# Kernel optimization log

Measured on AMD Instinct MI355X. Metric: run time of the kernel, lower is better.

## Reference

```python
import jax, jax.numpy as jnp
import numpy as np

N, DEG, FIN, HID, OUT = 50000, 16, 128, 128, 64


def setup_inputs() -> dict:
    key = jax.random.key(0)
    ks = jax.random.split(key, 32)
    x = jax.random.normal(ks[0], (N, FIN), dtype=jnp.float32)
    src = jax.random.randint(ks[1], (N * DEG,), 0, N, dtype=jnp.int32)
    dst = jnp.repeat(jnp.arange(N, dtype=jnp.int32), DEG)  # sorted by target, fixed degree
    edge_index = jnp.stack([src, dst])  # [2, E]
    dims = [(FIN, HID), (HID, HID), (HID, OUT)]
    params = {}
    i = 2
    for l, (fi, fo) in enumerate(dims, 1):
        s_lstm = 1.0 / np.sqrt(fi)
        params[f"W_ih{l}"] = jax.random.normal(ks[i + 0], (4 * fi, fi)) * s_lstm
        params[f"W_hh{l}"] = jax.random.normal(ks[i + 1], (4 * fi, fi)) * s_lstm
        params[f"b_ih{l}"] = jax.random.normal(ks[i + 2], (4 * fi,)) * s_lstm
        params[f"b_hh{l}"] = jax.random.normal(ks[i + 3], (4 * fi,)) * s_lstm
        params[f"Wl{l}"] = jax.random.normal(ks[i + 4], (fo, fi)) * (1.0 / np.sqrt(fi))
        params[f"bl{l}"] = jnp.zeros((fo,), jnp.float32)
        params[f"Wr{l}"] = jax.random.normal(ks[i + 5], (fo, fi)) * (1.0 / np.sqrt(fi))
        i += 6
    return {"x": x, "edge_index": edge_index, **params}


def _lstm_last(neigh, Wih, Whh, bih, bhh):
    # neigh: [N, deg, Fi]; PyTorch LSTM gate order i,f,g,o; return last-step output h.
    h0 = jnp.zeros((neigh.shape[0], Wih.shape[0] // 4), neigh.dtype)
    bias = bih + bhh

    def step(carry, xt):
        h, c = carry
        g = xt @ Wih.T + h @ Whh.T + bias
        i, f, gg, o = jnp.split(g, 4, axis=-1)
        c = jax.nn.sigmoid(f) * c + jax.nn.sigmoid(i) * jnp.tanh(gg)
        h = jax.nn.sigmoid(o) * jnp.tanh(c)
        return (h, c), None

    (h, _), _ = jax.lax.scan(step, (h0, h0), jnp.swapaxes(neigh, 0, 1))
    return h


def _sage_layer(x, src2d, Wih, Whh, bih, bhh, Wl, bl, Wr):
    neigh = x[src2d]  # gather: [N, deg, Fi]
    aggr = _lstm_last(neigh, Wih, Whh, bih, bhh)  # [N, Fi]
    return aggr @ Wl.T + bl + x @ Wr.T  # lin_l(aggr) + lin_r(x)


def reference(x, edge_index,
              W_ih1, W_hh1, b_ih1, b_hh1, Wl1, bl1, Wr1,
              W_ih2, W_hh2, b_ih2, b_hh2, Wl2, bl2, Wr2,
              W_ih3, W_hh3, b_ih3, b_hh3, Wl3, bl3, Wr3):
    n = x.shape[0]
    src2d = edge_index[0].reshape(n, -1)  # fixed-degree, dst-sorted edge list
    h = _sage_layer(x, src2d, W_ih1, W_hh1, b_ih1, b_hh1, Wl1, bl1, Wr1)
    h = jax.nn.relu(h)  # dropout is identity in eval mode
    h = _sage_layer(h, src2d, W_ih2, W_hh2, b_ih2, b_hh2, Wl2, bl2, Wr2)
    h = jax.nn.relu(h)
    return _sage_layer(h, src2d, W_ih3, W_hh3, b_ih3, b_hh3, Wl3, bl3, Wr3)
```

## Files before the change

### kernel.cpp

```cpp
#include <hip/hip_runtime.h>
#include <cstddef>
#include <cstdint>

typedef __attribute__((ext_vector_type(4))) float f32x4;
typedef __attribute__((ext_vector_type(8))) short short8;

#define HID 128
#define NK1 -1.4426950408889634f
#define PK2 2.8853900817779268f

#define BAR_LGKM() __asm__ volatile("s_waitcnt lgkmcnt(0)\ns_barrier" ::: "memory")
#define STEP_BAR2() __asm__ volatile("s_waitcnt vmcnt(2) lgkmcnt(0)\ns_barrier" ::: "memory")

__device__ __forceinline__ short f2bf(float f) {
  unsigned u = __builtin_bit_cast(unsigned, f);
  u += 0x7FFFu + ((u >> 16) & 1u);
  return (short)(u >> 16);
}
__device__ __forceinline__ unsigned pack_bf2(float a, float b) {
  unsigned ua = __builtin_bit_cast(unsigned, a) + 0x8000u;
  unsigned ub = __builtin_bit_cast(unsigned, b) + 0x8000u;
  return __builtin_amdgcn_perm(ub, ua, 0x07060302u);
}

__device__ __forceinline__ float lstm_elem(float si, float sf, float sg, float so, float& c) {
  float Ei = __builtin_amdgcn_exp2f(si);
  float Ef = __builtin_amdgcn_exp2f(sf);
  float Tg = __builtin_amdgcn_exp2f(sg);
  float Eo = __builtin_amdgcn_exp2f(so);
  float u = 1.0f + Ei, w = 1.0f + Ef, v = Tg + 1.0f, Tm = Tg - 1.0f;
  float t0 = u * v;
  float num = __builtin_fmaf(c, t0, w * Tm);
  float cn = num * __builtin_amdgcn_rcpf(w * t0);
  c = cn;
  float Tc = __builtin_amdgcn_exp2f(PK2 * cn);
  return (Tc - 1.0f) * __builtin_amdgcn_rcpf((1.0f + Eo) * (Tc + 1.0f));
}

__global__ void conv_x_kernel(const float* __restrict__ x, short* __restrict__ xb, int n,
                              int* __restrict__ tctr) {
  int i = blockIdx.x * blockDim.x + threadIdx.x;
  if (i < 8) tctr[i] = 0;
  int stride = gridDim.x * blockDim.x;
  for (; i < n; i += stride) xb[i] = f2bf(x[i]);
}

__global__ void conv_layer_kernel(const float* __restrict__ Wih, const float* __restrict__ Whh,
                                  const float* __restrict__ bih, const float* __restrict__ bhh,
                                  const float* __restrict__ Wl, const float* __restrict__ Wr, int foK,
                                  short* __restrict__ wihB, short* __restrict__ whhB,
                                  short* __restrict__ wlB, short* __restrict__ wrB,
                                  float* __restrict__ bsum) {
  int i = blockIdx.x * blockDim.x + threadIdx.x;
  if (i < 512 * HID) {
    float sc = ((i >> 14) == 2) ? PK2 : NK1;
    wihB[i] = f2bf(Wih[i] * sc);
    whhB[i] = f2bf(Whh[i] * sc);
  }
  if (i < foK) { wlB[i] = f2bf(Wl[i]); wrB[i] = f2bf(Wr[i]); }
  if (i < 512) bsum[i] = (bih[i] + bhh[i]) * (((i >> 7) == 2) ? PK2 : NK1);
}

#define ASTR 136
__global__ __launch_bounds__(512, 4) void pgemm_kernel(
    const short* __restrict__ A, const short* __restrict__ W,
    const float* __restrict__ bias, short* __restrict__ out, int M, int ntiles) {
  __shared__ short ldsA[32 * ASTR];
  const int tid = threadIdx.x;
  const int wave = tid >> 6, lane = tid & 63;
  const int quad = lane >> 4, nn = lane & 15;
  const int cbase = wave * 64;

  short8 wreg[4][4];
#pragma unroll
  for (int kt = 0; kt < 4; ++kt)
#pragma unroll
    for (int nt = 0; nt < 4; ++nt)
      wreg[kt][nt] = *(const short8*)(W + (size_t)(cbase + nt * 16 + nn) * HID + kt * 32 + quad * 8);
  f32x4 bias4[4];
#pragma unroll
  for (int nt = 0; nt < 4; ++nt)
#pragma unroll
    for (int r = 0; r < 4; ++r) bias4[nt][r] = bias[cbase + nt * 16 + quad * 4 + r];

  const int srow = wave * 4 + quad;
  const int scol = nn * 8;

  int rt = blockIdx.x;
  short8 avn;
  {
    int r = rt * 32 + srow;
    if (r > M - 1) r = M - 1;
    avn = *(const short8*)(A + (size_t)r * HID + scol);
  }

#pragma unroll 1
  for (; rt < ntiles; rt += gridDim.x) {
    const int row0 = rt * 32;
    BAR_LGKM();
    *(short8*)(ldsA + srow * ASTR + scol) = avn;
    {
      int rn = rt + gridDim.x;
      if (rn < ntiles) {
        int r = rn * 32 + srow;
        if (r > M - 1) r = M - 1;
        avn = *(const short8*)(A + (size_t)r * HID + scol);
      }
    }
    BAR_LGKM();

    f32x4 acc[2][4];
#pragma unroll
    for (int b = 0; b < 2; ++b)
#pragma unroll
      for (int nt = 0; nt < 4; ++nt) acc[b][nt] = bias4[nt];
#pragma unroll
    for (int kt = 0; kt < 4; ++kt) {
      short8 af0 = *(const short8*)(ldsA + nn * ASTR + kt * 32 + quad * 8);
      short8 af1 = *(const short8*)(ldsA + (16 + nn) * ASTR + kt * 32 + quad * 8);
#pragma unroll
      for (int nt = 0; nt < 4; ++nt) {
        acc[0][nt] = __builtin_amdgcn_mfma_f32_16x16x32_bf16(wreg[kt][nt], af0, acc[0][nt], 0, 0, 0);
        acc[1][nt] = __builtin_amdgcn_mfma_f32_16x16x32_bf16(wreg[kt][nt], af1, acc[1][nt], 0, 0, 0);
      }
    }

#pragma unroll
    for (int b = 0; b < 2; ++b) {
      int row = row0 + b * 16 + nn;
      if (row < M) {
#pragma unroll
        for (int nt = 0; nt < 4; ++nt) {
          uint2 pk;
          pk.x = pack_bf2(acc[b][nt][0], acc[b][nt][1]);
          pk.y = pack_bf2(acc[b][nt][2], acc[b][nt][3]);
          *(uint2*)(out + (size_t)row * 512 + cbase + nt * 16 + quad * 4) = pk;
        }
      }
    }
  }
}

#define NPB 16
#define PSTR 520
#define HSTR 152
#define LSTM_LDS_BYTES ((3 * NPB * PSTR + 2 * NPB * HSTR) * 2 + 256 * 4 + 16)

template <int FO, bool RELU, bool OUTF32>
__global__ __launch_bounds__(512, 4) void lstm_fused_kernel(
    const short* __restrict__ P, const short* __restrict__ Whh,
    const int* __restrict__ src, const short* __restrict__ cur,
    const short* __restrict__ Wl, const short* __restrict__ Wr,
    const float* __restrict__ bl,
    short* __restrict__ outB, float* __restrict__ outF, int M, int ntiles,
    int* __restrict__ tctr) {
  extern __shared__ char smem[];
  short* Pb = (short*)smem;
  short* Hb = Pb + 3 * NPB * PSTR;
  int* srcL = (int*)(Hb + 2 * NPB * HSTR);
  int* nextTp = srcL + 256;

  const int tid = threadIdx.x;
  const int wave = tid >> 6, lane = tid & 63;
  const int quad = lane >> 4, nn = lane & 15;
  const int r0row = wave * 2, r1row = wave * 2 + 1;
  const char* Pbase = (const char*)P + lane * 16;

  short8 wreg[4][4];
#pragma unroll
  for (int kt = 0; kt < 4; ++kt)
#pragma unroll
    for (int q = 0; q < 4; ++q)
      wreg[kt][q] = *(const short8*)(Whh + (size_t)(q * 128 + wave * 16 + nn) * HID + kt * 32 + quad * 8);

  short8 ident;
#pragma unroll
  for (int e = 0; e < 8; ++e) ident[e] = (short)((quad * 8 + e == nn) ? 0x3F80 : 0);
  f32x4 zero4 = {0.f, 0.f, 0.f, 0.f};
  __asm__ volatile("" : "+v"(zero4));

  int tile = blockIdx.x;
  while (tile < ntiles) {
    const int nodeBase = tile * NPB;
    if (tid < 256) {
      int node = nodeBase + (tid >> 4);
      srcL[tid] = ((node < M) ? src[nodeBase * 16 + tid] : 0) << 10;
    }
    if (tid == 0) *nextTp = (int)gridDim.x + atomicAdd(tctr, 1);
    float c_st[4] = {0.f, 0.f, 0.f, 0.f};
    BAR_LGKM();
    const int my_next = *nextTp;

    {
      int s0A = srcL[r0row * 16 + 0], s0B = srcL[r1row * 16 + 0];
      __builtin_amdgcn_global_load_lds(
          (const __attribute__((address_space(1))) unsigned int*)(Pbase + s0A),
          (__attribute__((address_space(3))) unsigned int*)(Pb + r0row * PSTR), 16, 0, 0);
      __builtin_amdgcn_global_load_lds(
          (const __attribute__((address_space(1))) unsigned int*)(Pbase + s0B),
          (__attribute__((address_space(3))) unsigned int*)(Pb + r1row * PSTR), 16, 0, 0);
      int s1A = srcL[r0row * 16 + 1], s1B = srcL[r1row * 16 + 1];
      __builtin_amdgcn_global_load_lds(
          (const __attribute__((address_space(1))) unsigned int*)(Pbase + s1A),
          (__attribute__((address_space(3))) unsigned int*)(Pb + NPB * PSTR + r0row * PSTR), 16, 0, 0);
      __builtin_amdgcn_global_load_lds(
          (const __attribute__((address_space(1))) unsigned int*)(Pbase + s1B),
          (__attribute__((address_space(3))) unsigned int*)(Pb + NPB * PSTR + r1row * PSTR), 16, 0, 0);
    }
    int sA = srcL[r0row * 16 + 2], sB = srcL[r1row * 16 + 2];

    int pc = 0, pg = 2;
#pragma unroll 1
    for (int t = 0; t < 16; ++t) {
      short* Pc = Pb + pc * NPB * PSTR;
      short* Pg = Pb + pg * NPB * PSTR;
      const short* Hp = Hb + ((t + 1) & 1) * NPB * HSTR;
      short* Hw = Hb + (t & 1) * NPB * HSTR;
      pc = (pc == 2) ? 0 : pc + 1;
      pg = (pg == 2) ? 0 : pg + 1;

      STEP_BAR2();

      const short* pB = Pc + nn * PSTR + wave * 16 + (quad & 1) * 8;
      short8 pf0 = *(const short8*)(pB + 0 * 128);
      short8 pf1 = *(const short8*)(pB + 1 * 128);
      short8 pf2 = *(const short8*)(pB + 2 * 128);
      short8 pf3 = *(const short8*)(pB + 3 * 128);

      __builtin_amdgcn_global_load_lds(
          (const __attribute__((address_space(1))) unsigned int*)(Pbase + sA),
          (__attribute__((address_space(3))) unsigned int*)(Pg + r0row * PSTR), 16, 0, 0);
      __builtin_amdgcn_global_load_lds(
          (const __attribute__((address_space(1))) unsigned int*)(Pbase + sB),
          (__attribute__((address_space(3))) unsigned int*)(Pg + r1row * PSTR), 16, 0, 0);
      {
        int tn = (t + 3 < 16) ? t + 3 : 15;
        sA = srcL[r0row * 16 + tn];
        sB = srcL[r1row * 16 + tn];
      }

      f32x4 acc[4];
      acc[0] = __builtin_amdgcn_mfma_f32_16x16x32_bf16(ident, pf0, zero4, 0, 0, 0);
      acc[1] = __builtin_amdgcn_mfma_f32_16x16x32_bf16(ident, pf1, zero4, 0, 0, 0);
      acc[2] = __builtin_amdgcn_mfma_f32_16x16x32_bf16(ident, pf2, zero4, 0, 0, 0);
      acc[3] = __builtin_amdgcn_mfma_f32_16x16x32_bf16(ident, pf3, zero4, 0, 0, 0);

      if (t) {
#pragma unroll
        for (int kt = 0; kt < 4; ++kt) {
          short8 hb = *(const short8*)(Hp + nn * HSTR + kt * 32 + quad * 8);
#pragma unroll
          for (int q = 0; q < 4; ++q)
            acc[q] = __builtin_amdgcn_mfma_f32_16x16x32_bf16(wreg[kt][q], hb, acc[q], 0, 0, 0);
        }
      }

      float hv[4];
#pragma unroll
      for (int r = 0; r < 4; ++r)
        hv[r] = lstm_elem(acc[0][r], acc[1][r], acc[2][r], acc[3][r], c_st[r]);
      uint2 pk;
      pk.x = pack_bf2(hv[0], hv[1]);
      pk.y = pack_bf2(hv[2], hv[3]);
      *(uint2*)(Hw + nn * HSTR + wave * 16 + quad * 4) = pk;
    }

    BAR_LGKM();

    if (FO == 128 || wave < 4) {
      const short* Hf = Hb + NPB * HSTR;
      const int cbase = wave * 16;
      f32x4 accO;
#pragma unroll
      for (int r = 0; r < 4; ++r) accO[r] = bl[cbase + quad * 4 + r];
#pragma unroll
      for (int kt = 0; kt < 4; ++kt) {
        short8 wlA = *(const short8*)(Wl + (size_t)(cbase + nn) * HID + kt * 32 + quad * 8);
        short8 hb = *(const short8*)(Hf + nn * HSTR + kt * 32 + quad * 8);
        accO = __builtin_amdgcn_mfma_f32_16x16x32_bf16(wlA, hb, accO, 0, 0, 0);
        short8 wrA = *(const short8*)(Wr + (size_t)(cbase + nn) * HID + kt * 32 + quad * 8);
        short8 cb = *(const short8*)(cur + (size_t)(nodeBase + nn) * HID + kt * 32 + quad * 8);
        accO = __builtin_amdgcn_mfma_f32_16x16x32_bf16(wrA, cb, accO, 0, 0, 0);
      }
      if (RELU) {
#pragma unroll
        for (int r = 0; r < 4; ++r) accO[r] = fmaxf(accO[r], 0.0f);
      }
      int node = nodeBase + nn;
      if (node < M) {
        if (OUTF32) {
          *(f32x4*)(outF + (size_t)node * FO + cbase + quad * 4) = accO;
        } else {
          uint2 pko;
          pko.x = pack_bf2(accO[0], accO[1]);
          pko.y = pack_bf2(accO[2], accO[3]);
          *(uint2*)(outB + (size_t)node * FO + cbase + quad * 4) = pko;
        }
      }
    }
    tile = my_next;
  }
}

extern "C" void kernel_launch(void* const* d_in, const int* in_sizes, int n_in,
                              void* d_out, int out_size, void* d_ws, size_t ws_size,
                              hipStream_t stream) {
  const float* x = (const float*)d_in[0];
  const int* src = (const int*)d_in[1];
  const float* Wih[3] = {(const float*)d_in[2], (const float*)d_in[9], (const float*)d_in[16]};
  const float* Whh[3] = {(const float*)d_in[3], (const float*)d_in[10], (const float*)d_in[17]};
  const float* bih[3] = {(const float*)d_in[4], (const float*)d_in[11], (const float*)d_in[18]};
  const float* bhh[3] = {(const float*)d_in[5], (const float*)d_in[12], (const float*)d_in[19]};
  const float* Wl[3]  = {(const float*)d_in[6], (const float*)d_in[13], (const float*)d_in[20]};
  const float* bl[3]  = {(const float*)d_in[7], (const float*)d_in[14], (const float*)d_in[21]};
  const float* Wr[3]  = {(const float*)d_in[8], (const float*)d_in[15], (const float*)d_in[22]};

  const int M = in_sizes[0] / HID;

  char* ws = (char*)d_ws;
  size_t off = 0;
  auto alloc = [&](size_t bytes) -> void* {
    void* p = ws + off;
    off += (bytes + 255) & ~(size_t)255;
    return p;
  };
  short* curA = (short*)alloc((size_t)M * HID * 2);
  short* curB = (short*)alloc((size_t)M * HID * 2);
  short* Pbuf = (short*)alloc((size_t)M * 512 * 2);
  short* wihB[3]; short* whhB[3]; short* wlB[3]; short* wrB[3]; float* bsum[3];
  for (int l = 0; l < 3; ++l) {
    wihB[l] = (short*)alloc(512 * HID * 2);
    whhB[l] = (short*)alloc(512 * HID * 2);
    wlB[l]  = (short*)alloc(HID * HID * 2);
    wrB[l]  = (short*)alloc(HID * HID * 2);
    bsum[l] = (float*)alloc(512 * 4);
  }
  int* tctr = (int*)alloc(256);

  const int nltiles = (M + NPB - 1) / NPB;
  const int ntiles = (M + 31) / 32;

  (void)hipFuncSetAttribute((const void*)lstm_fused_kernel<128, true, false>,
                            hipFuncAttributeMaxDynamicSharedMemorySize, LSTM_LDS_BYTES);
  (void)hipFuncSetAttribute((const void*)lstm_fused_kernel<64, false, true>,
                            hipFuncAttributeMaxDynamicSharedMemorySize, LSTM_LDS_BYTES);

  conv_x_kernel<<<2048, 256, 0, stream>>>(x, curA, M * HID, tctr);
  for (int l = 0; l < 3; ++l) {
    const int Fo = (l == 2) ? 64 : 128;
    conv_layer_kernel<<<256, 256, 0, stream>>>(Wih[l], Whh[l], bih[l], bhh[l], Wl[l], Wr[l],
                                               Fo * HID, wihB[l], whhB[l], wlB[l], wrB[l], bsum[l]);
  }

  short* cur = curA;
  short* nxt = curB;
  for (int l = 0; l < 3; ++l) {
    pgemm_kernel<<<784, 512, 0, stream>>>(cur, wihB[l], bsum[l], Pbuf, M, ntiles);
    if (l < 2) {
      lstm_fused_kernel<128, true, false><<<512, 512, LSTM_LDS_BYTES, stream>>>(
          Pbuf, whhB[l], src, cur, wlB[l], wrB[l], bl[l], nxt, nullptr, M, nltiles, tctr + l);
      short* tswap = cur; cur = nxt; nxt = tswap;
    } else {
      lstm_fused_kernel<64, false, true><<<512, 512, LSTM_LDS_BYTES, stream>>>(
          Pbuf, whhB[l], src, cur, wlB[l], wrB[l], bl[l], nullptr, (float*)d_out, M, nltiles, tctr + 2);
    }
  }
}
```

Before: 741.3 us.

## Fuse all conversion, GEMM and LSTM stages into one cooperative persistent kernel

Replaces the sequence of conversion, input-projection GEMM and fused LSTM kernel launches with a single cooperative kernel that uses grid-wide syncs between phases. The input GEMM phase also switches to atomic-counter dynamic tile scheduling and stages bias in LDS. The aim is to remove per-launch overhead and tail gaps between kernels. The cost is grid.sync overhead and grid size being tied to occupancy, with the old multi-kernel path kept as a fallback if the cooperative launch fails.

```diff
diff --git a/kernel.cpp b/kernel.cpp
--- a/kernel.cpp
+++ b/kernel.cpp
@@ -1,6 +1,9 @@
 #include <hip/hip_runtime.h>
+#include <hip/hip_cooperative_groups.h>
 #include <cstddef>
 #include <cstdint>
+
+namespace cg = cooperative_groups;
 
 typedef __attribute__((ext_vector_type(4))) float f32x4;
 typedef __attribute__((ext_vector_type(8))) short short8;
@@ -37,6 +40,296 @@
   return (Tc - 1.0f) * __builtin_amdgcn_rcpf((1.0f + Eo) * (Tc + 1.0f));
 }
 
+#define ASTR 136
+#define NPB 16
+#define PSTR 520
+#define HSTR 152
+#define LSTM_LDS_BYTES ((3 * NPB * PSTR + 2 * NPB * HSTR) * 2 + 256 * 4 + 16)
+
+struct KParams {
+  const float* x;
+  const int* src;
+  const float* Wih[3]; const float* Whh[3];
+  const float* bih[3]; const float* bhh[3];
+  const float* Wl[3];  const float* bl[3]; const float* Wr[3];
+  short* curA; short* curB; short* Pbuf;
+  short* wihB[3]; short* whhB[3]; short* wlB[3]; short* wrB[3];
+  float* bsum[3];
+  int* tctr;
+  float* outF;
+  int M, ntiles, nltiles;
+};
+
+__global__ __launch_bounds__(512, 4) void fused_all(KParams p) {
+  extern __shared__ char smem[];
+  const int tid = threadIdx.x;
+  const int wave = tid >> 6, lane = tid & 63;
+  const int quad = lane >> 4, nn = lane & 15;
+  cg::grid_group grid = cg::this_grid();
+
+  {
+    const int gi = blockIdx.x * 512 + tid;
+    const int gs = (int)gridDim.x * 512;
+    if (gi < 8) p.tctr[gi] = 0;
+    const int nx = p.M * HID;
+    for (int i = gi; i < nx; i += gs) p.curA[i] = f2bf(p.x[i]);
+#pragma unroll 1
+    for (int l = 0; l < 3; ++l) {
+      const int foK = ((l == 2) ? 64 : 128) * HID;
+      for (int i = gi; i < 512 * HID; i += gs) {
+        float sc = ((i >> 14) == 2) ? PK2 : NK1;
+        p.wihB[l][i] = f2bf(p.Wih[l][i] * sc);
+        p.whhB[l][i] = f2bf(p.Whh[l][i] * sc);
+      }
+      for (int i = gi; i < foK; i += gs) {
+        p.wlB[l][i] = f2bf(p.Wl[l][i]);
+        p.wrB[l][i] = f2bf(p.Wr[l][i]);
+      }
+      for (int i = gi; i < 512; i += gs)
+        p.bsum[l][i] = (p.bih[l][i] + p.bhh[l][i]) * (((i >> 7) == 2) ? PK2 : NK1);
+    }
+  }
+  grid.sync();
+
+  short* cur = p.curA;
+  short* nxt = p.curB;
+
+#pragma unroll 1
+  for (int l = 0; l < 3; ++l) {
+    {
+      short* ldsA = (short*)smem;
+      float* ldsB = (float*)(smem + 32 * ASTR * 2);
+      int* nextTp = (int*)(ldsB + 512);
+      const short* A = cur;
+      const short* W = p.wihB[l];
+      short* outP = p.Pbuf;
+      int* ctr = p.tctr + 3 + l;
+      const int Mloc = p.M, ntl = p.ntiles;
+      const int cbase = wave * 64;
+      const int srow = wave * 4 + quad;
+      const int scol = nn * 8;
+
+      short8 wreg[4][4];
+#pragma unroll
+      for (int kt = 0; kt < 4; ++kt)
+#pragma unroll
+        for (int nt = 0; nt < 4; ++nt)
+          wreg[kt][nt] = *(const short8*)(W + (size_t)(cbase + nt * 16 + nn) * HID + kt * 32 + quad * 8);
+      ldsB[tid] = p.bsum[l][tid];
+
+      int rt = blockIdx.x;
+      short8 avn;
+      {
+        int r = rt * 32 + srow;
+        if (r > Mloc - 1) r = Mloc - 1;
+        avn = *(const short8*)(A + (size_t)r * HID + scol);
+      }
+#pragma unroll 1
+      while (rt < ntl) {
+        if (tid == 0) *nextTp = (int)gridDim.x + atomicAdd(ctr, 1);
+        BAR_LGKM();
+        *(short8*)(ldsA + srow * ASTR + scol) = avn;
+        const int rn = *nextTp;
+        if (rn < ntl) {
+          int r = rn * 32 + srow;
+          if (r > Mloc - 1) r = Mloc - 1;
+          avn = *(const short8*)(A + (size_t)r * HID + scol);
+        }
+        BAR_LGKM();
+        f32x4 acc[2][4];
+#pragma unroll
+        for (int nt = 0; nt < 4; ++nt) {
+          f32x4 bv = *(const f32x4*)(ldsB + cbase + nt * 16 + quad * 4);
+          acc[0][nt] = bv;
+          acc[1][nt] = bv;
+        }
+#pragma unroll
+        for (int kt = 0; kt < 4; ++kt) {
+          short8 af0 = *(const short8*)(ldsA + nn * ASTR + kt * 32 + quad * 8);
+          short8 af1 = *(const short8*)(ldsA + (16 + nn) * ASTR + kt * 32 + quad * 8);
+#pragma unroll
+          for (int nt = 0; nt < 4; ++nt) {
+            acc[0][nt] = __builtin_amdgcn_mfma_f32_16x16x32_bf16(wreg[kt][nt], af0, acc[0][nt], 0, 0, 0);
+            acc[1][nt] = __builtin_amdgcn_mfma_f32_16x16x32_bf16(wreg[kt][nt], af1, acc[1][nt], 0, 0, 0);
+          }
+        }
+        const int row0 = rt * 32;
+#pragma unroll
+        for (int b = 0; b < 2; ++b) {
+          int row = row0 + b * 16 + nn;
+          if (row < Mloc) {
+#pragma unroll
+            for (int nt = 0; nt < 4; ++nt) {
+              uint2 pk;
+              pk.x = pack_bf2(acc[b][nt][0], acc[b][nt][1]);
+              pk.y = pack_bf2(acc[b][nt][2], acc[b][nt][3]);
+              *(uint2*)(outP + (size_t)row * 512 + cbase + nt * 16 + quad * 4) = pk;
+            }
+          }
+        }
+        rt = rn;
+      }
+    }
+    grid.sync();
+
+    {
+      short* Pb = (short*)smem;
+      short* Hb = Pb + 3 * NPB * PSTR;
+      int* srcL = (int*)(Hb + 2 * NPB * HSTR);
+      int* nextTp = srcL + 256;
+      const short* Whh = p.whhB[l];
+      const short* Wlw = p.wlB[l];
+      const short* Wrw = p.wrB[l];
+      const float* blw = p.bl[l];
+      int* ctr = p.tctr + l;
+      const int Mloc = p.M, ntl = p.nltiles;
+      const int r0row = wave * 2, r1row = wave * 2 + 1;
+      const char* Pbase = (const char*)p.Pbuf + lane * 16;
+      const int FO = (l == 2) ? 64 : 128;
+
+      short8 wreg[4][4];
+#pragma unroll
+      for (int kt = 0; kt < 4; ++kt)
+#pragma unroll
+        for (int q = 0; q < 4; ++q)
+          wreg[kt][q] = *(const short8*)(Whh + (size_t)(q * 128 + wave * 16 + nn) * HID + kt * 32 + quad * 8);
+
+      short8 ident;
+#pragma unroll
+      for (int e = 0; e < 8; ++e) ident[e] = (short)((quad * 8 + e == nn) ? 0x3F80 : 0);
+      f32x4 zero4 = {0.f, 0.f, 0.f, 0.f};
+      __asm__ volatile("" : "+v"(zero4));
+
+      int tile = blockIdx.x;
+#pragma unroll 1
+      while (tile < ntl) {
+        const int nodeBase = tile * NPB;
+        if (tid < 256) {
+          int node = nodeBase + (tid >> 4);
+          srcL[tid] = ((node < Mloc) ? p.src[nodeBase * 16 + tid] : 0) << 10;
+        }
+        if (tid == 0) *nextTp = (int)gridDim.x + atomicAdd(ctr, 1);
+        float c_st[4] = {0.f, 0.f, 0.f, 0.f};
+        BAR_LGKM();
+        const int my_next = *nextTp;
+
+        {
+          int s0A = srcL[r0row * 16 + 0], s0B = srcL[r1row * 16 + 0];
+          __builtin_amdgcn_global_load_lds(
+              (const __attribute__((address_space(1))) unsigned int*)(Pbase + s0A),
+              (__attribute__((address_space(3))) unsigned int*)(Pb + r0row * PSTR), 16, 0, 0);
+          __builtin_amdgcn_global_load_lds(
+              (const __attribute__((address_space(1))) unsigned int*)(Pbase + s0B),
+              (__attribute__((address_space(3))) unsigned int*)(Pb + r1row * PSTR), 16, 0, 0);
+          int s1A = srcL[r0row * 16 + 1], s1B = srcL[r1row * 16 + 1];
+          __builtin_amdgcn_global_load_lds(
+              (const __attribute__((address_space(1))) unsigned int*)(Pbase + s1A),
+              (__attribute__((address_space(3))) unsigned int*)(Pb + NPB * PSTR + r0row * PSTR), 16, 0, 0);
+          __builtin_amdgcn_global_load_lds(
+              (const __attribute__((address_space(1))) unsigned int*)(Pbase + s1B),
+              (__attribute__((address_space(3))) unsigned int*)(Pb + NPB * PSTR + r1row * PSTR), 16, 0, 0);
+        }
+        int sA = srcL[r0row * 16 + 2], sB = srcL[r1row * 16 + 2];
+
+        int pc = 0, pg = 2;
+#pragma unroll 1
+        for (int t = 0; t < 16; ++t) {
+          short* Pc = Pb + pc * NPB * PSTR;
+          short* Pg = Pb + pg * NPB * PSTR;
+          const short* Hp = Hb + ((t + 1) & 1) * NPB * HSTR;
+          short* Hw = Hb + (t & 1) * NPB * HSTR;
+          pc = (pc == 2) ? 0 : pc + 1;
+          pg = (pg == 2) ? 0 : pg + 1;
+
+          STEP_BAR2();
+
+          const short* pB = Pc + nn * PSTR + wave * 16 + (quad & 1) * 8;
+          short8 pf0 = *(const short8*)(pB + 0 * 128);
+          short8 pf1 = *(const short8*)(pB + 1 * 128);
+          short8 pf2 = *(const short8*)(pB + 2 * 128);
+          short8 pf3 = *(const short8*)(pB + 3 * 128);
+
+          __builtin_amdgcn_global_load_lds(
+              (const __attribute__((address_space(1))) unsigned int*)(Pbase + sA),
+              (__attribute__((address_space(3))) unsigned int*)(Pg + r0row * PSTR), 16, 0, 0);
+          __builtin_amdgcn_global_load_lds(
+              (const __attribute__((address_space(1))) unsigned int*)(Pbase + sB),
+              (__attribute__((address_space(3))) unsigned int*)(Pg + r1row * PSTR), 16, 0, 0);
+          {
+            int tn = (t + 3 < 16) ? t + 3 : 15;
+            sA = srcL[r0row * 16 + tn];
+            sB = srcL[r1row * 16 + tn];
+          }
+
+          f32x4 acc[4];
+          acc[0] = __builtin_amdgcn_mfma_f32_16x16x32_bf16(ident, pf0, zero4, 0, 0, 0);
+          acc[1] = __builtin_amdgcn_mfma_f32_16x16x32_bf16(ident, pf1, zero4, 0, 0, 0);
+          acc[2] = __builtin_amdgcn_mfma_f32_16x16x32_bf16(ident, pf2, zero4, 0, 0, 0);
+          acc[3] = __builtin_amdgcn_mfma_f32_16x16x32_bf16(ident, pf3, zero4, 0, 0, 0);
+
+          if (t) {
+#pragma unroll
+            for (int kt = 0; kt < 4; ++kt) {
+              short8 hb = *(const short8*)(Hp + nn * HSTR + kt * 32 + quad * 8);
+#pragma unroll
+              for (int q = 0; q < 4; ++q)
+                acc[q] = __builtin_amdgcn_mfma_f32_16x16x32_bf16(wreg[kt][q], hb, acc[q], 0, 0, 0);
+            }
+          }
+
+          float hv[4];
+#pragma unroll
+          for (int r = 0; r < 4; ++r)
+            hv[r] = lstm_elem(acc[0][r], acc[1][r], acc[2][r], acc[3][r], c_st[r]);
+          uint2 pk;
+          pk.x = pack_bf2(hv[0], hv[1]);
+          pk.y = pack_bf2(hv[2], hv[3]);
+          *(uint2*)(Hw + nn * HSTR + wave * 16 + quad * 4) = pk;
+        }
+
+        BAR_LGKM();
+
+        if (FO == 128 || wave < 4) {
+          const short* Hf = Hb + NPB * HSTR;
+          const int cbase = wave * 16;
+          f32x4 accO;
+#pragma unroll
+          for (int r = 0; r < 4; ++r) accO[r] = blw[cbase + quad * 4 + r];
+#pragma unroll
+          for (int kt = 0; kt < 4; ++kt) {
+            short8 wlA = *(const short8*)(Wlw + (size_t)(cbase + nn) * HID + kt * 32 + quad * 8);
+            short8 hb = *(const short8*)(Hf + nn * HSTR + kt * 32 + quad * 8);
+            accO = __builtin_amdgcn_mfma_f32_16x16x32_bf16(wlA, hb, accO, 0, 0, 0);
+            short8 wrA = *(const short8*)(Wrw + (size_t)(cbase + nn) * HID + kt * 32 + quad * 8);
+            short8 cb = *(const short8*)(cur + (size_t)(nodeBase + nn) * HID + kt * 32 + quad * 8);
+            accO = __builtin_amdgcn_mfma_f32_16x16x32_bf16(wrA, cb, accO, 0, 0, 0);
+          }
+          if (l < 2) {
+#pragma unroll
+            for (int r = 0; r < 4; ++r) accO[r] = fmaxf(accO[r], 0.0f);
+          }
+          int node = nodeBase + nn;
+          if (node < Mloc) {
+            if (l == 2) {
+              *(f32x4*)(p.outF + (size_t)node * 64 + cbase + quad * 4) = accO;
+            } else {
+              uint2 pko;
+              pko.x = pack_bf2(accO[0], accO[1]);
+              pko.y = pack_bf2(accO[2], accO[3]);
+              *(uint2*)(nxt + (size_t)node * 128 + cbase + quad * 4) = pko;
+            }
+          }
+        }
+        tile = my_next;
+      }
+    }
+    if (l < 2) {
+      grid.sync();
+      short* t = cur; cur = nxt; nxt = t;
+    }
+  }
+}
+
 __global__ void conv_x_kernel(const float* __restrict__ x, short* __restrict__ xb, int n,
                               int* __restrict__ tctr) {
   int i = blockIdx.x * blockDim.x + threadIdx.x;
@@ -61,7 +354,6 @@
   if (i < 512) bsum[i] = (bih[i] + bhh[i]) * (((i >> 7) == 2) ? PK2 : NK1);
 }
 
-#define ASTR 136
 __global__ __launch_bounds__(512, 4) void pgemm_kernel(
     const short* __restrict__ A, const short* __restrict__ W,
     const float* __restrict__ bias, short* __restrict__ out, int M, int ntiles) {
@@ -70,7 +362,6 @@
   const int wave = tid >> 6, lane = tid & 63;
   const int quad = lane >> 4, nn = lane & 15;
   const int cbase = wave * 64;
-
   short8 wreg[4][4];
 #pragma unroll
   for (int kt = 0; kt < 4; ++kt)
@@ -82,10 +373,8 @@
   for (int nt = 0; nt < 4; ++nt)
 #pragma unroll
     for (int r = 0; r < 4; ++r) bias4[nt][r] = bias[cbase + nt * 16 + quad * 4 + r];
-
   const int srow = wave * 4 + quad;
   const int scol = nn * 8;
-
   int rt = blockIdx.x;
   short8 avn;
   {
@@ -93,7 +382,6 @@
     if (r > M - 1) r = M - 1;
     avn = *(const short8*)(A + (size_t)r * HID + scol);
   }
-
 #pragma unroll 1
   for (; rt < ntiles; rt += gridDim.x) {
     const int row0 = rt * 32;
@@ -108,7 +396,6 @@
       }
     }
     BAR_LGKM();
-
     f32x4 acc[2][4];
 #pragma unroll
     for (int b = 0; b < 2; ++b)
@@ -124,7 +411,6 @@
         acc[1][nt] = __builtin_amdgcn_mfma_f32_16x16x32_bf16(wreg[kt][nt], af1, acc[1][nt], 0, 0, 0);
       }
     }
-
 #pragma unroll
     for (int b = 0; b < 2; ++b) {
       int row = row0 + b * 16 + nn;
@@ -140,11 +426,6 @@
     }
   }
 }
-
-#define NPB 16
-#define PSTR 520
-#define HSTR 152
-#define LSTM_LDS_BYTES ((3 * NPB * PSTR + 2 * NPB * HSTR) * 2 + 256 * 4 + 16)
 
 template <int FO, bool RELU, bool OUTF32>
 __global__ __launch_bounds__(512, 4) void lstm_fused_kernel(
@@ -159,26 +440,22 @@
   short* Hb = Pb + 3 * NPB * PSTR;
   int* srcL = (int*)(Hb + 2 * NPB * HSTR);
   int* nextTp = srcL + 256;
-
   const int tid = threadIdx.x;
   const int wave = tid >> 6, lane = tid & 63;
   const int quad = lane >> 4, nn = lane & 15;
   const int r0row = wave * 2, r1row = wave * 2 + 1;
   const char* Pbase = (const char*)P + lane * 16;
-
   short8 wreg[4][4];
 #pragma unroll
   for (int kt = 0; kt < 4; ++kt)
 #pragma unroll
     for (int q = 0; q < 4; ++q)
       wreg[kt][q] = *(const short8*)(Whh + (size_t)(q * 128 + wave * 16 + nn) * HID + kt * 32 + quad * 8);
-
   short8 ident;
 #pragma unroll
   for (int e = 0; e < 8; ++e) ident[e] = (short)((quad * 8 + e == nn) ? 0x3F80 : 0);
   f32x4 zero4 = {0.f, 0.f, 0.f, 0.f};
   __asm__ volatile("" : "+v"(zero4));
-
   int tile = blockIdx.x;
   while (tile < ntiles) {
     const int nodeBase = tile * NPB;
@@ -190,7 +467,6 @@
     float c_st[4] = {0.f, 0.f, 0.f, 0.f};
     BAR_LGKM();
     const int my_next = *nextTp;
-
     {
       int s0A = srcL[r0row * 16 + 0], s0B = srcL[r1row * 16 + 0];
       __builtin_amdgcn_global_load_lds(
@@ -208,7 +484,6 @@
           (__attribute__((address_space(3))) unsigned int*)(Pb + NPB * PSTR + r1row * PSTR), 16, 0, 0);
     }
     int sA = srcL[r0row * 16 + 2], sB = srcL[r1row * 16 + 2];
-
     int pc = 0, pg = 2;
 #pragma unroll 1
     for (int t = 0; t < 16; ++t) {
@@ -218,15 +493,12 @@
       short* Hw = Hb + (t & 1) * NPB * HSTR;
       pc = (pc == 2) ? 0 : pc + 1;
       pg = (pg == 2) ? 0 : pg + 1;
-
       STEP_BAR2();
-
       const short* pB = Pc + nn * PSTR + wave * 16 + (quad & 1) * 8;
       short8 pf0 = *(const short8*)(pB + 0 * 128);
       short8 pf1 = *(const short8*)(pB + 1 * 128);
       short8 pf2 = *(const short8*)(pB + 2 * 128);
       short8 pf3 = *(const short8*)(pB + 3 * 128);
-
       __builtin_amdgcn_global_load_lds(
           (const __attribute__((address_space(1))) unsigned int*)(Pbase + sA),
           (__attribute__((address_space(3))) unsigned int*)(Pg + r0row * PSTR), 16, 0, 0);
@@ -238,13 +510,11 @@
         sA = srcL[r0row * 16 + tn];
         sB = srcL[r1row * 16 + tn];
       }
-
       f32x4 acc[4];
       acc[0] = __builtin_amdgcn_mfma_f32_16x16x32_bf16(ident, pf0, zero4, 0, 0, 0);
       acc[1] = __builtin_amdgcn_mfma_f32_16x16x32_bf16(ident, pf1, zero4, 0, 0, 0);
       acc[2] = __builtin_amdgcn_mfma_f32_16x16x32_bf16(ident, pf2, zero4, 0, 0, 0);
       acc[3] = __builtin_amdgcn_mfma_f32_16x16x32_bf16(ident, pf3, zero4, 0, 0, 0);
-
       if (t) {
 #pragma unroll
         for (int kt = 0; kt < 4; ++kt) {
@@ -254,7 +524,6 @@
             acc[q] = __builtin_amdgcn_mfma_f32_16x16x32_bf16(wreg[kt][q], hb, acc[q], 0, 0, 0);
         }
       }
-
       float hv[4];
 #pragma unroll
       for (int r = 0; r < 4; ++r)
@@ -264,9 +533,7 @@
       pk.y = pack_bf2(hv[2], hv[3]);
       *(uint2*)(Hw + nn * HSTR + wave * 16 + quad * 4) = pk;
     }
-
     BAR_LGKM();
-
     if (FO == 128 || wave < 4) {
       const short* Hf = Hb + NPB * HSTR;
       const int cbase = wave * 16;
@@ -340,29 +607,61 @@
   const int nltiles = (M + NPB - 1) / NPB;
   const int ntiles = (M + 31) / 32;
 
-  (void)hipFuncSetAttribute((const void*)lstm_fused_kernel<128, true, false>,
+  (void)hipFuncSetAttribute((const void*)fused_all,
                             hipFuncAttributeMaxDynamicSharedMemorySize, LSTM_LDS_BYTES);
-  (void)hipFuncSetAttribute((const void*)lstm_fused_kernel<64, false, true>,
-                            hipFuncAttributeMaxDynamicSharedMemorySize, LSTM_LDS_BYTES);
-
-  conv_x_kernel<<<2048, 256, 0, stream>>>(x, curA, M * HID, tctr);
+
+  int dev = 0;
+  (void)hipGetDevice(&dev);
+  int ncu = 256;
+  (void)hipDeviceGetAttribute(&ncu, hipDeviceAttributeMultiprocessorCount, dev);
+  int occB = 0;
+  (void)hipOccupancyMaxActiveBlocksPerMultiprocessor(&occB, (const void*)fused_all, 512,
+                                                     LSTM_LDS_BYTES);
+  if (occB < 1) occB = 1;
+  long grid = (long)occB * (long)ncu;
+  if (grid > 512) grid = 512;
+
+  KParams kp;
+  kp.x = x; kp.src = src;
   for (int l = 0; l < 3; ++l) {
-    const int Fo = (l == 2) ? 64 : 128;
-    conv_layer_kernel<<<256, 256, 0, stream>>>(Wih[l], Whh[l], bih[l], bhh[l], Wl[l], Wr[l],
-                                               Fo * HID, wihB[l], whhB[l], wlB[l], wrB[l], bsum[l]);
-  }
-
-  short* cur = curA;
-  short* nxt = curB;
-  for (int l = 0; l < 3; ++l) {
-    pgemm_kernel<<<784, 512, 0, stream>>>(cur, wihB[l], bsum[l], Pbuf, M, ntiles);
-    if (l < 2) {
-      lstm_fused_kernel<128, true, false><<<512, 512, LSTM_LDS_BYTES, stream>>>(
-          Pbuf, whhB[l], src, cur, wlB[l], wrB[l], bl[l], nxt, nullptr, M, nltiles, tctr + l);
-      short* tswap = cur; cur = nxt; nxt = tswap;
-    } else {
-      lstm_fused_kernel<64, false, true><<<512, 512, LSTM_LDS_BYTES, stream>>>(
-          Pbuf, whhB[l], src, cur, wlB[l], wrB[l], bl[l], nullptr, (float*)d_out, M, nltiles, tctr + 2);
-    }
-  }
-}
+    kp.Wih[l] = Wih[l]; kp.Whh[l] = Whh[l];
+    kp.bih[l] = bih[l]; kp.bhh[l] = bhh[l];
+    kp.Wl[l] = Wl[l]; kp.bl[l] = bl[l]; kp.Wr[l] = Wr[l];
+    kp.wihB[l] = wihB[l]; kp.whhB[l] = whhB[l];
+    kp.wlB[l] = wlB[l]; kp.wrB[l] = wrB[l];
+    kp.bsum[l] = bsum[l];
+  }
+  kp.curA = curA; kp.curB = curB; kp.Pbuf = Pbuf;
+  kp.tctr = tctr; kp.outF = (float*)d_out;
+  kp.M = M; kp.ntiles = ntiles; kp.nltiles = nltiles;
+
+  void* kargs[] = {(void*)&kp};
+  hipError_t le = hipLaunchCooperativeKernel((const void*)fused_all, dim3((unsigned)grid),
+                                             dim3(512), kargs, (unsigned)LSTM_LDS_BYTES, stream);
+  if (le != hipSuccess) {
+    (void)hipFuncSetAttribute((const void*)lstm_fused_kernel<128, true, false>,
+                              hipFuncAttributeMaxDynamicSharedMemorySize, LSTM_LDS_BYTES);
+    (void)hipFuncSetAttribute((const void*)lstm_fused_kernel<64, false, true>,
+                              hipFuncAttributeMaxDynamicSharedMemorySize, LSTM_LDS_BYTES);
+    conv_x_kernel<<<2048, 256, 0, stream>>>(x, curA, M * HID, tctr);
+    for (int l = 0; l < 3; ++l) {
+      const int Fo = (l == 2) ? 64 : 128;
+      conv_layer_kernel<<<256, 256, 0, stream>>>(Wih[l], Whh[l], bih[l], bhh[l], Wl[l], Wr[l],
+                                                 Fo * HID, wihB[l], whhB[l], wlB[l], wrB[l], bsum[l]);
+    }
+    short* cur = curA;
+    short* nxt = curB;
+    for (int l = 0; l < 3; ++l) {
+      pgemm_kernel<<<784, 512, 0, stream>>>(cur, wihB[l], bsum[l], Pbuf, M, ntiles);
+      if (l < 2) {
+        lstm_fused_kernel<128, true, false><<<512, 512, LSTM_LDS_BYTES, stream>>>(
+            Pbuf, whhB[l], src, cur, wlB[l], wrB[l], bl[l], nxt, nullptr, M, nltiles, tctr + l);
+        short* tswap = cur; cur = nxt; nxt = tswap;
+      } else {
+        lstm_fused_kernel<64, false, true><<<512, 512, LSTM_LDS_BYTES, stream>>>(
+            Pbuf, whhB[l], src, cur, wlB[l], wrB[l], bl[l], nullptr, (float*)d_out, M, nltiles,
+            tctr + 2);
+      }
+    }
+  }
+}
```

New measurement: 1.195 ms. 61.2% more time.
